# Performance work log

Measured on AMD Instinct MI355X. Metric: run time of the kernel, lower is better.

## Reference

```python
import jax, jax.numpy as jnp
import numpy as np

D = 1024          # feature_dim
ROT = D // 2      # rotary applied to first feature_dim//2 channels (RotaryEmbedding(dim//2))
B, S = 4, 8192


def _l2norm(x, eps=1e-6):
    # cos_sim feature map: x / ||x||_2 along feature dim
    return x * jax.lax.rsqrt(jnp.sum(x * x, axis=-1, keepdims=True) + eps)


def _rotary(x, rot_dim):
    # lucidrains rotary-embedding-torch: interleaved pairs, partial rotary on first rot_dim dims
    seq = x.shape[-2]
    half = rot_dim // 2
    inv_freq = 1.0 / (10000.0 ** (jnp.arange(0, rot_dim, 2, dtype=jnp.float32) / rot_dim))  # [rot/2]
    freqs = jnp.arange(seq, dtype=jnp.float32)[:, None] * inv_freq[None, :]                  # [s, rot/2]
    freqs = jnp.repeat(freqs, 2, axis=-1)                                                     # [s, rot]
    cos, sin = jnp.cos(freqs), jnp.sin(freqs)
    xr, xp = x[..., :rot_dim], x[..., rot_dim:]
    x2 = xr.reshape(*xr.shape[:-1], half, 2)
    rh = jnp.stack([-x2[..., 1], x2[..., 0]], axis=-1).reshape(xr.shape)  # rotate_half, interleaved
    return jnp.concatenate([xr * cos + rh * sin, xp], axis=-1)


def _layernorm(x, g, b, eps=1e-5):
    mu = jnp.mean(x, axis=-1, keepdims=True)
    var = jnp.mean(jnp.square(x - mu), axis=-1, keepdims=True)
    return (x - mu) * jax.lax.rsqrt(var + eps) * g + b


def setup_inputs() -> dict:
    key = jax.random.key(0)
    k1, k2, k3 = jax.random.split(key, 3)
    X = jax.random.normal(k1, (B, S, D), jnp.float32)
    W_in = jax.random.normal(k2, (3 * D, D), jnp.float32) / np.float32(np.sqrt(D))
    W_out = jax.random.normal(k3, (D, D), jnp.float32) / np.float32(np.sqrt(D))
    ln_g = jnp.ones((D,), jnp.float32)
    ln_b = jnp.zeros((D,), jnp.float32)
    return {"X": X, "W_in": W_in, "W_out": W_out, "ln_g": ln_g, "ln_b": ln_b}


def reference(X, W_in, W_out, ln_g, ln_b):
    Xn = _layernorm(X, ln_g, ln_b)
    QKV = jnp.einsum('bsd,ed->bse', Xn, W_in)        # in_proj, no bias
    Q, K, V = jnp.split(QKV, 3, axis=-1)
    Q = _rotary(Q, ROT)
    K = _rotary(K, ROT)
    A = jnp.sum(_l2norm(K) * V, axis=-2)             # [b, d] global feature-map reduction
    Y = A[:, None, :] * _l2norm(Q)                   # feature_map_attn = identity
    Y = jnp.einsum('bsd,ed->bse', Y, W_out)          # out_proj, no bias
    return Y + X                                     # residual
```

## Files before the change

kernel.cpp:

```cpp
#include <hip/hip_runtime.h>

#define D 1024
#define S_LEN 8192
#define BATCH 4
#define NROWS (BATCH * S_LEN)

typedef unsigned short u16;
typedef __attribute__((ext_vector_type(8))) short short8;
typedef __attribute__((ext_vector_type(8))) unsigned short u16x8;
typedef __attribute__((ext_vector_type(4))) unsigned short u16x4;
typedef __attribute__((ext_vector_type(4))) float f32x4;

__device__ __forceinline__ float bf2f(u16 u) {
  return __builtin_bit_cast(float, ((unsigned)u) << 16);
}
__device__ __forceinline__ u16 f2bf(float f) {
  unsigned u = __builtin_bit_cast(unsigned, f);
  u += 0x7FFFu + ((u >> 16) & 1u);
  return (u16)(u >> 16);
}

#define GLD16(gp, lp)                                                    \
  __builtin_amdgcn_global_load_lds(                                      \
      (__attribute__((address_space(1))) void*)(void*)(gp),              \
      (__attribute__((address_space(3))) void*)(void*)(lp), 16, 0, 0)

__global__ __launch_bounds__(256) void prep_kernel(
    const float* __restrict__ X, const float* __restrict__ g,
    const float* __restrict__ bb, u16* __restrict__ Xn,
    float* __restrict__ ct, float* __restrict__ st,
    const float* __restrict__ Wa, u16* __restrict__ da, int n4a,
    const float* __restrict__ Wb, u16* __restrict__ db, int n4b) {
  const int bid = blockIdx.x;
  const int tid = threadIdx.x;
  if (bid < 8192) {
    const int wave = tid >> 6, lane = tid & 63;
    const int row = bid * 4 + wave;
    const float* xr = X + (size_t)row * D;
    float4 v[4];
    float s = 0.f, sq = 0.f;
#pragma unroll
    for (int i = 0; i < 4; i++) {
      v[i] = *(const float4*)&xr[lane * 4 + i * 256];
      s += v[i].x + v[i].y + v[i].z + v[i].w;
      sq += v[i].x * v[i].x + v[i].y * v[i].y + v[i].z * v[i].z + v[i].w * v[i].w;
    }
#pragma unroll
    for (int off = 32; off > 0; off >>= 1) {
      s += __shfl_xor(s, off);
      sq += __shfl_xor(sq, off);
    }
    const float mu = s * (1.f / D);
    const float var = sq * (1.f / D) - mu * mu;
    const float rstd = rsqrtf(var + 1e-5f);
#pragma unroll
    for (int i = 0; i < 4; i++) {
      const int c = lane * 4 + i * 256;
      float4 gg = *(const float4*)&g[c];
      float4 bv = *(const float4*)&bb[c];
      u16x4 o;
      o[0] = f2bf((v[i].x - mu) * rstd * gg.x + bv.x);
      o[1] = f2bf((v[i].y - mu) * rstd * gg.y + bv.y);
      o[2] = f2bf((v[i].z - mu) * rstd * gg.z + bv.z);
      o[3] = f2bf((v[i].w - mu) * rstd * gg.w + bv.w);
      *(u16x4*)&Xn[(size_t)row * D + c] = o;
    }
  } else if (bid < 16384) {
    const int t = (bid - 8192) * 256 + tid;
    const int s = t >> 8, j = t & 255;
    const float invf = exp2f((float)j * -0.0519051265f);
    const float f = (float)s * invf;
    float rev = f * 0.15915494309189535f;
    rev -= floorf(rev);
    ct[t] = cospif(2.f * rev);
    st[t] = sinpif(2.f * rev);
  } else {
    int t = (bid - 16384) * 256 + tid;
    const float* sp;
    u16* d;
    if (t < n4a) {
      sp = Wa + (size_t)t * 4;
      d = da + (size_t)t * 4;
    } else {
      t -= n4a;
      if (t >= n4b) return;
      sp = Wb + (size_t)t * 4;
      d = db + (size_t)t * 4;
    }
    float4 v = *(const float4*)sp;
    u16x4 o;
    o[0] = f2bf(v.x); o[1] = f2bf(v.y); o[2] = f2bf(v.z); o[3] = f2bf(v.w);
    *(u16x4*)d = o;
  }
}

template <int EPI>
__global__ __launch_bounds__(256) void gemm_bt(
    const u16* __restrict__ A, const u16* __restrict__ Bm,
    u16* __restrict__ Cbf, const float* __restrict__ Xres,
    float* __restrict__ Cf, int K, int ldc) {
  __shared__ u16 smem[2 * 128 * 64];
  u16* As = smem;
  u16* Bs = smem + 128 * 64;
  const int tid = threadIdx.x;
  const int wave = tid >> 6, lane = tid & 63;
  const int wm = wave >> 1, wn = wave & 1;
  const int l15 = lane & 15, quad = lane >> 4;
  const int m0 = blockIdx.y * 128;
  const int n0 = blockIdx.x * 128;
  const int sw = l15 & 7;

  f32x4 acc[4][4] = {};

  for (int k0 = 0; k0 < K; k0 += 64) {
    __syncthreads();
#pragma unroll
    for (int i = 0; i < 4; i++) {
      const int c = i * 256 + tid;
      const int row = c >> 3;
      const int g = (c & 7) ^ (row & 7);
      GLD16(&A[(size_t)(m0 + row) * K + k0 + g * 8], &As[c * 8]);
      GLD16(&Bm[(size_t)(n0 + row) * K + k0 + g * 8], &Bs[c * 8]);
    }
    __syncthreads();
#pragma unroll
    for (int ks = 0; ks < 2; ks++) {
      short8 af[4], bfr[4];
#pragma unroll
      for (int i = 0; i < 4; i++)
        af[i] = *(const short8*)
            &As[(wm * 64 + i * 16 + l15) * 64 + (((ks * 4 + quad) ^ sw) << 3)];
#pragma unroll
      for (int j = 0; j < 4; j++)
        bfr[j] = *(const short8*)
            &Bs[(wn * 64 + j * 16 + l15) * 64 + (((ks * 4 + quad) ^ sw) << 3)];
#pragma unroll
      for (int i = 0; i < 4; i++)
#pragma unroll
        for (int j = 0; j < 4; j++)
          acc[i][j] = __builtin_amdgcn_mfma_f32_16x16x32_bf16(
              af[i], bfr[j], acc[i][j], 0, 0, 0);
    }
  }

  if constexpr (EPI == 0) {
    __syncthreads();
    u16* my = smem + wave * 4096;
#pragma unroll
    for (int i = 0; i < 4; i++)
#pragma unroll
      for (int j = 0; j < 4; j++)
#pragma unroll
        for (int r = 0; r < 4; r++)
          my[(i * 16 + quad * 4 + r) * 64 + j * 16 + l15] = f2bf(acc[i][j][r]);
    __syncthreads();
#pragma unroll
    for (int t = 0; t < 8; t++) {
      const int flat = t * 512 + lane * 8;
      const int r64 = flat >> 6, c64 = flat & 63;
      *(u16x8*)&Cbf[(size_t)(m0 + wm * 64 + r64) * ldc + n0 + wn * 64 + c64] =
          *(const u16x8*)&my[flat];
    }
  } else {
#pragma unroll
    for (int i = 0; i < 4; i++) {
#pragma unroll
      for (int r = 0; r < 4; r++) {
        const int row = m0 + wm * 64 + i * 16 + quad * 4 + r;
#pragma unroll
        for (int j = 0; j < 4; j++) {
          const int col = n0 + wn * 64 + j * 16 + l15;
          Cf[(size_t)row * ldc + col] =
              acc[i][j][r] + Xres[(size_t)row * ldc + col];
        }
      }
    }
  }
}

__global__ __launch_bounds__(256) void areduce_kernel(
    const u16* __restrict__ QKV, const float* __restrict__ ct,
    const float* __restrict__ st, float* __restrict__ Apart) {
  const int wave = threadIdx.x >> 6, lane = threadIdx.x & 63;
  const int b = blockIdx.x >> 8;
  const int chunk = blockIdx.x & 255;
  const int c0 = lane << 4;
  float acc[16];
#pragma unroll
  for (int i = 0; i < 16; i++) acc[i] = 0.f;

  for (int t = 0; t < 8; t++) {
    const int s = chunk * 32 + wave * 8 + t;
    const size_t base = ((size_t)b * S_LEN + s) * (3 * D);
    u16x8 ka = *(const u16x8*)&QKV[base + D + c0];
    u16x8 kb = *(const u16x8*)&QKV[base + D + c0 + 8];
    float kx[16];
#pragma unroll
    for (int i = 0; i < 8; i++) { kx[i] = bf2f(ka[i]); kx[8 + i] = bf2f(kb[i]); }
    if (lane < 32) {
      const int jb = c0 >> 1;
      const float* cp = &ct[(size_t)s * 256 + jb];
      const float* sp = &st[(size_t)s * 256 + jb];
#pragma unroll
      for (int p = 0; p < 8; p++) {
        float cv = cp[p], sv = sp[p];
        float e = kx[2 * p], o = kx[2 * p + 1];
        kx[2 * p] = e * cv - o * sv;
        kx[2 * p + 1] = o * cv + e * sv;
      }
    }
    float sq = 0.f;
#pragma unroll
    for (int i = 0; i < 16; i++) sq += kx[i] * kx[i];
#pragma unroll
    for (int off = 32; off > 0; off >>= 1) sq += __shfl_xor(sq, off);
    const float rn = rsqrtf(sq + 1e-6f);
    u16x8 va = *(const u16x8*)&QKV[base + 2 * D + c0];
    u16x8 vb = *(const u16x8*)&QKV[base + 2 * D + c0 + 8];
#pragma unroll
    for (int i = 0; i < 8; i++) {
      acc[i] += kx[i] * rn * bf2f(va[i]);
      acc[8 + i] += kx[8 + i] * rn * bf2f(vb[i]);
    }
  }

  __shared__ float red[4][D];
#pragma unroll
  for (int i = 0; i < 4; i++)
    *(float4*)&red[wave][c0 + i * 4] =
        make_float4(acc[i * 4], acc[i * 4 + 1], acc[i * 4 + 2], acc[i * 4 + 3]);
  __syncthreads();
  const int tid = threadIdx.x;
  float4 s0 = *(const float4*)&red[0][tid * 4];
  float4 s1 = *(const float4*)&red[1][tid * 4];
  float4 s2 = *(const float4*)&red[2][tid * 4];
  float4 s3 = *(const float4*)&red[3][tid * 4];
  float4 o;
  o.x = s0.x + s1.x + s2.x + s3.x;
  o.y = s0.y + s1.y + s2.y + s3.y;
  o.z = s0.z + s1.z + s2.z + s3.z;
  o.w = s0.w + s1.w + s2.w + s3.w;
  *(float4*)&Apart[((size_t)blockIdx.x << 10) + tid * 4] = o;
}

__global__ __launch_bounds__(256) void afinal_kernel(
    const float* __restrict__ Apart, float* __restrict__ Aout) {
  const int e = blockIdx.x * 256 + threadIdx.x;
  const int b = e >> 10, d = e & 1023;
  const float* p = Apart + ((size_t)b << 18) + d;
  float s = 0.f;
#pragma unroll 8
  for (int c = 0; c < 256; c++) s += p[(size_t)c << 10];
  Aout[e] = s;
}

__global__ __launch_bounds__(256) void y_kernel(
    const u16* __restrict__ QKV, const float* __restrict__ ct,
    const float* __restrict__ st, const float* __restrict__ Ain,
    u16* __restrict__ Y) {
  const int wave = threadIdx.x >> 6, lane = threadIdx.x & 63;
  const int row = blockIdx.x * 4 + wave;
  const int b = row >> 13, s = row & (S_LEN - 1);
  const int c0 = lane << 4;
  const size_t base = (size_t)row * (3 * D);
  u16x8 qa = *(const u16x8*)&QKV[base + c0];
  u16x8 qb = *(const u16x8*)&QKV[base + c0 + 8];
  float qx[16];
#pragma unroll
  for (int i = 0; i < 8; i++) { qx[i] = bf2f(qa[i]); qx[8 + i] = bf2f(qb[i]); }
  if (lane < 32) {
    const int jb = c0 >> 1;
    const float* cp = &ct[(size_t)s * 256 + jb];
    const float* sp = &st[(size_t)s * 256 + jb];
#pragma unroll
    for (int p = 0; p < 8; p++) {
      float cv = cp[p], sv = sp[p];
      float e = qx[2 * p], o = qx[2 * p + 1];
      qx[2 * p] = e * cv - o * sv;
      qx[2 * p + 1] = o * cv + e * sv;
    }
  }
  float sq = 0.f;
#pragma unroll
  for (int i = 0; i < 16; i++) sq += qx[i] * qx[i];
#pragma unroll
  for (int off = 32; off > 0; off >>= 1) sq += __shfl_xor(sq, off);
  const float rn = rsqrtf(sq + 1e-6f);
  u16x8 oa, ob;
#pragma unroll
  for (int i = 0; i < 8; i++) {
    oa[i] = f2bf(Ain[(b << 10) + c0 + i] * qx[i] * rn);
    ob[i] = f2bf(Ain[(b << 10) + c0 + 8 + i] * qx[8 + i] * rn);
  }
  *(u16x8*)&Y[(size_t)row * D + c0] = oa;
  *(u16x8*)&Y[(size_t)row * D + c0 + 8] = ob;
}

extern "C" void kernel_launch(void* const* d_in, const int* in_sizes, int n_in,
                              void* d_out, int out_size, void* d_ws, size_t ws_size,
                              hipStream_t stream) {
  const float* X = (const float*)d_in[0];
  const float* W_in = (const float*)d_in[1];
  const float* W_out = (const float*)d_in[2];
  const float* ln_g = (const float*)d_in[3];
  const float* ln_b = (const float*)d_in[4];
  float* out = (float*)d_out;

  char* ws = (char*)d_ws;
  size_t off = 0;
  auto alloc = [&](size_t bytes) -> void* {
    void* p = ws + off;
    off += (bytes + 255) & ~(size_t)255;
    return p;
  };
  u16* QKV = (u16*)alloc((size_t)NROWS * 3 * D * 2);
  u16* Xn = (u16*)alloc((size_t)NROWS * D * 2);
  u16* Yb = (u16*)alloc((size_t)NROWS * D * 2);
  u16* Winb = (u16*)alloc((size_t)3 * D * D * 2);
  u16* Woutb = (u16*)alloc((size_t)D * D * 2);
  float* ct = (float*)alloc((size_t)S_LEN * 256 * 4);
  float* st = (float*)alloc((size_t)S_LEN * 256 * 4);
  float* Apart = (float*)alloc((size_t)BATCH * 256 * D * 4);
  float* Aacc = (float*)alloc((size_t)BATCH * D * 4);

  const int n4a = 3 * D * D / 4, n4b = D * D / 4;
  prep_kernel<<<20480, 256, 0, stream>>>(X, ln_g, ln_b, Xn, ct, st, W_in, Winb,
                                         n4a, W_out, Woutb, n4b);

  dim3 g1(3 * D / 128, NROWS / 128);
  gemm_bt<0><<<g1, 256, 0, stream>>>(Xn, Winb, QKV, nullptr, nullptr, D, 3 * D);

  areduce_kernel<<<BATCH * 256, 256, 0, stream>>>(QKV, ct, st, Apart);
  afinal_kernel<<<16, 256, 0, stream>>>(Apart, Aacc);
  y_kernel<<<NROWS / 4, 256, 0, stream>>>(QKV, ct, st, Aacc, Yb);

  dim3 g2(D / 128, NROWS / 128);
  gemm_bt<1><<<g2, 256, 0, stream>>>(Yb, Woutb, nullptr, X, out, D, D);
}
```

Baseline: 650.5 us.

## Run QKV projection GEMM in FP8 with scaled MFMA instead of bf16

LayerNorm output and W_in (pre-scaled by 16) are quantized to FP8 in the prep kernel, and the input projection uses a new GEMM built on the mfma_scale 16x16x128 f8f6f4 instruction, with a scale exponent that undoes the ×16. This halves operand bytes and doubles the MFMA K per instruction for the largest GEMM. The out-projection GEMM stays in bf16. The cost is reduced precision in Q/K/V, which could threaten tolerance.

```diff
diff --git a/kernel.cpp b/kernel.cpp
--- a/kernel.cpp
+++ b/kernel.cpp
@@ -10,6 +10,8 @@
 typedef __attribute__((ext_vector_type(8))) unsigned short u16x8;
 typedef __attribute__((ext_vector_type(4))) unsigned short u16x4;
 typedef __attribute__((ext_vector_type(4))) float f32x4;
+typedef __attribute__((ext_vector_type(4))) int int4v;
+typedef __attribute__((ext_vector_type(8))) int int8v;
 
 __device__ __forceinline__ float bf2f(u16 u) {
   return __builtin_bit_cast(float, ((unsigned)u) << 16);
@@ -19,6 +21,12 @@
   u += 0x7FFFu + ((u >> 16) & 1u);
   return (u16)(u >> 16);
 }
+__device__ __forceinline__ int pk_fp8x4(float a, float b, float c, float d) {
+  int v = 0;
+  v = __builtin_amdgcn_cvt_pk_fp8_f32(a, b, v, false);
+  v = __builtin_amdgcn_cvt_pk_fp8_f32(c, d, v, true);
+  return v;
+}
 
 #define GLD16(gp, lp)                                                    \
   __builtin_amdgcn_global_load_lds(                                      \
@@ -27,9 +35,9 @@
 
 __global__ __launch_bounds__(256) void prep_kernel(
     const float* __restrict__ X, const float* __restrict__ g,
-    const float* __restrict__ bb, u16* __restrict__ Xn,
+    const float* __restrict__ bb, unsigned char* __restrict__ Xn8,
     float* __restrict__ ct, float* __restrict__ st,
-    const float* __restrict__ Wa, u16* __restrict__ da, int n4a,
+    const float* __restrict__ Wa, unsigned char* __restrict__ da8, int n4a,
     const float* __restrict__ Wb, u16* __restrict__ db, int n4b) {
   const int bid = blockIdx.x;
   const int tid = threadIdx.x;
@@ -58,12 +66,11 @@
       const int c = lane * 4 + i * 256;
       float4 gg = *(const float4*)&g[c];
       float4 bv = *(const float4*)&bb[c];
-      u16x4 o;
-      o[0] = f2bf((v[i].x - mu) * rstd * gg.x + bv.x);
-      o[1] = f2bf((v[i].y - mu) * rstd * gg.y + bv.y);
-      o[2] = f2bf((v[i].z - mu) * rstd * gg.z + bv.z);
-      o[3] = f2bf((v[i].w - mu) * rstd * gg.w + bv.w);
-      *(u16x4*)&Xn[(size_t)row * D + c] = o;
+      int p = pk_fp8x4((v[i].x - mu) * rstd * gg.x + bv.x,
+                       (v[i].y - mu) * rstd * gg.y + bv.y,
+                       (v[i].z - mu) * rstd * gg.z + bv.z,
+                       (v[i].w - mu) * rstd * gg.w + bv.w);
+      *(int*)&Xn8[(size_t)row * D + c] = p;
     }
   } else if (bid < 16384) {
     const int t = (bid - 8192) * 256 + tid;
@@ -74,31 +81,98 @@
     rev -= floorf(rev);
     ct[t] = cospif(2.f * rev);
     st[t] = sinpif(2.f * rev);
+  } else if (bid < 19456) {
+    const int t = (bid - 16384) * 256 + tid;
+    if (t < n4a) {
+      float4 v = *(const float4*)&Wa[(size_t)t * 4];
+      *(int*)&da8[(size_t)t * 4] =
+          pk_fp8x4(v.x * 16.f, v.y * 16.f, v.z * 16.f, v.w * 16.f);
+    }
   } else {
-    int t = (bid - 16384) * 256 + tid;
-    const float* sp;
-    u16* d;
-    if (t < n4a) {
-      sp = Wa + (size_t)t * 4;
-      d = da + (size_t)t * 4;
-    } else {
-      t -= n4a;
-      if (t >= n4b) return;
-      sp = Wb + (size_t)t * 4;
-      d = db + (size_t)t * 4;
-    }
-    float4 v = *(const float4*)sp;
-    u16x4 o;
-    o[0] = f2bf(v.x); o[1] = f2bf(v.y); o[2] = f2bf(v.z); o[3] = f2bf(v.w);
-    *(u16x4*)d = o;
-  }
-}
-
-template <int EPI>
+    const int t = (bid - 19456) * 256 + tid;
+    if (t < n4b) {
+      float4 v = *(const float4*)&Wb[(size_t)t * 4];
+      u16x4 o;
+      o[0] = f2bf(v.x); o[1] = f2bf(v.y); o[2] = f2bf(v.z); o[3] = f2bf(v.w);
+      *(u16x4*)&db[(size_t)t * 4] = o;
+    }
+  }
+}
+
+__global__ __launch_bounds__(256) void gemm_fp8(
+    const unsigned char* __restrict__ A8, const unsigned char* __restrict__ B8,
+    u16* __restrict__ Cbf, int K, int ldc) {
+  __shared__ unsigned char smem[2 * 128 * 128];
+  unsigned char* As = smem;
+  unsigned char* Bs = smem + 128 * 128;
+  const int tid = threadIdx.x;
+  const int wave = tid >> 6, lane = tid & 63;
+  const int wm = wave >> 1, wn = wave & 1;
+  const int l15 = lane & 15, quad = lane >> 4;
+  const int m0 = blockIdx.y * 128;
+  const int n0 = blockIdx.x * 128;
+  const int sw = l15 & 7;
+
+  f32x4 acc[4][4] = {};
+
+  for (int k0 = 0; k0 < K; k0 += 128) {
+    __syncthreads();
+#pragma unroll
+    for (int i = 0; i < 4; i++) {
+      const int c = i * 256 + tid;
+      const int row = c >> 3;
+      const int g = (c & 7) ^ (row & 7);
+      GLD16(&A8[(size_t)(m0 + row) * K + k0 + g * 16], &As[c * 16]);
+      GLD16(&B8[(size_t)(n0 + row) * K + k0 + g * 16], &Bs[c * 16]);
+    }
+    __syncthreads();
+    int8v af[4], bfr[4];
+#pragma unroll
+    for (int i = 0; i < 4; i++) {
+      const int ro = (wm * 64 + i * 16 + l15) * 128;
+      int4v lo = *(const int4v*)&As[ro + (((quad * 2) ^ sw) << 4)];
+      int4v hi = *(const int4v*)&As[ro + (((quad * 2 + 1) ^ sw) << 4)];
+      af[i][0] = lo[0]; af[i][1] = lo[1]; af[i][2] = lo[2]; af[i][3] = lo[3];
+      af[i][4] = hi[0]; af[i][5] = hi[1]; af[i][6] = hi[2]; af[i][7] = hi[3];
+    }
+#pragma unroll
+    for (int j = 0; j < 4; j++) {
+      const int ro = (wn * 64 + j * 16 + l15) * 128;
+      int4v lo = *(const int4v*)&Bs[ro + (((quad * 2) ^ sw) << 4)];
+      int4v hi = *(const int4v*)&Bs[ro + (((quad * 2 + 1) ^ sw) << 4)];
+      bfr[j][0] = lo[0]; bfr[j][1] = lo[1]; bfr[j][2] = lo[2]; bfr[j][3] = lo[3];
+      bfr[j][4] = hi[0]; bfr[j][5] = hi[1]; bfr[j][6] = hi[2]; bfr[j][7] = hi[3];
+    }
+#pragma unroll
+    for (int i = 0; i < 4; i++)
+#pragma unroll
+      for (int j = 0; j < 4; j++)
+        acc[i][j] = __builtin_amdgcn_mfma_scale_f32_16x16x128_f8f6f4(
+            af[i], bfr[j], acc[i][j], 0, 0, 0, 0x7F7F7F7F, 0, 0x7B7B7B7B);
+  }
+
+  __syncthreads();
+  u16* my = (u16*)smem + wave * 4096;
+#pragma unroll
+  for (int i = 0; i < 4; i++)
+#pragma unroll
+    for (int j = 0; j < 4; j++)
+#pragma unroll
+      for (int r = 0; r < 4; r++)
+        my[(i * 16 + quad * 4 + r) * 64 + j * 16 + l15] = f2bf(acc[i][j][r]);
+  __syncthreads();
+#pragma unroll
+  for (int t = 0; t < 8; t++) {
+    const int flat = t * 512 + lane * 8;
+    const int r64 = flat >> 6, c64 = flat & 63;
+    *(u16x8*)&Cbf[(size_t)(m0 + wm * 64 + r64) * ldc + n0 + wn * 64 + c64] =
+        *(const u16x8*)&my[flat];
+  }
+}
+
 __global__ __launch_bounds__(256) void gemm_bt(
     const u16* __restrict__ A, const u16* __restrict__ Bm,
-    u16* __restrict__ Cbf, const float* __restrict__ Xres,
-    float* __restrict__ Cf, int K, int ldc) {
+    const float* __restrict__ Xres, float* __restrict__ Cf, int K, int ldc) {
   __shared__ u16 smem[2 * 128 * 64];
   u16* As = smem;
   u16* Bs = smem + 128 * 64;
@@ -143,36 +217,16 @@
     }
   }
 
-  if constexpr (EPI == 0) {
-    __syncthreads();
-    u16* my = smem + wave * 4096;
-#pragma unroll
-    for (int i = 0; i < 4; i++)
-#pragma unroll
-      for (int j = 0; j < 4; j++)
-#pragma unroll
-        for (int r = 0; r < 4; r++)
-          my[(i * 16 + quad * 4 + r) * 64 + j * 16 + l15] = f2bf(acc[i][j][r]);
-    __syncthreads();
-#pragma unroll
-    for (int t = 0; t < 8; t++) {
-      const int flat = t * 512 + lane * 8;
-      const int r64 = flat >> 6, c64 = flat & 63;
-      *(u16x8*)&Cbf[(size_t)(m0 + wm * 64 + r64) * ldc + n0 + wn * 64 + c64] =
-          *(const u16x8*)&my[flat];
-    }
-  } else {
-#pragma unroll
-    for (int i = 0; i < 4; i++) {
-#pragma unroll
-      for (int r = 0; r < 4; r++) {
-        const int row = m0 + wm * 64 + i * 16 + quad * 4 + r;
-#pragma unroll
-        for (int j = 0; j < 4; j++) {
-          const int col = n0 + wn * 64 + j * 16 + l15;
-          Cf[(size_t)row * ldc + col] =
-              acc[i][j][r] + Xres[(size_t)row * ldc + col];
-        }
+#pragma unroll
+  for (int i = 0; i < 4; i++) {
+#pragma unroll
+    for (int r = 0; r < 4; r++) {
+      const int row = m0 + wm * 64 + i * 16 + quad * 4 + r;
+#pragma unroll
+      for (int j = 0; j < 4; j++) {
+        const int col = n0 + wn * 64 + j * 16 + l15;
+        Cf[(size_t)row * ldc + col] =
+            acc[i][j][r] + Xres[(size_t)row * ldc + col];
       }
     }
   }
@@ -314,9 +368,9 @@
     return p;
   };
   u16* QKV = (u16*)alloc((size_t)NROWS * 3 * D * 2);
-  u16* Xn = (u16*)alloc((size_t)NROWS * D * 2);
+  unsigned char* Xn8 = (unsigned char*)alloc((size_t)NROWS * D);
   u16* Yb = (u16*)alloc((size_t)NROWS * D * 2);
-  u16* Winb = (u16*)alloc((size_t)3 * D * D * 2);
+  unsigned char* Win8 = (unsigned char*)alloc((size_t)3 * D * D);
   u16* Woutb = (u16*)alloc((size_t)D * D * 2);
   float* ct = (float*)alloc((size_t)S_LEN * 256 * 4);
   float* st = (float*)alloc((size_t)S_LEN * 256 * 4);
@@ -324,16 +378,16 @@
   float* Aacc = (float*)alloc((size_t)BATCH * D * 4);
 
   const int n4a = 3 * D * D / 4, n4b = D * D / 4;
-  prep_kernel<<<20480, 256, 0, stream>>>(X, ln_g, ln_b, Xn, ct, st, W_in, Winb,
+  prep_kernel<<<20480, 256, 0, stream>>>(X, ln_g, ln_b, Xn8, ct, st, W_in, Win8,
                                          n4a, W_out, Woutb, n4b);
 
   dim3 g1(3 * D / 128, NROWS / 128);
-  gemm_bt<0><<<g1, 256, 0, stream>>>(Xn, Winb, QKV, nullptr, nullptr, D, 3 * D);
+  gemm_fp8<<<g1, 256, 0, stream>>>(Xn8, Win8, QKV, D, 3 * D);
 
   areduce_kernel<<<BATCH * 256, 256, 0, stream>>>(QKV, ct, st, Apart);
   afinal_kernel<<<16, 256, 0, stream>>>(Apart, Aacc);
   y_kernel<<<NROWS / 4, 256, 0, stream>>>(QKV, ct, st, Aacc, Yb);
 
   dim3 g2(D / 128, NROWS / 128);
-  gemm_bt<1><<<g2, 256, 0, stream>>>(Yb, Woutb, nullptr, X, out, D, D);
-}
+  gemm_bt<<<g2, 256, 0, stream>>>(Yb, Woutb, X, out, D, D);
+}
```

Result: faster. 537.9 us (-17.3%).
